# Optimization experiments

Hardware: AMD Instinct MI355X
Metric: run time of the kernel (lower is better)

The kernel has to match this reference:

```python
import jax, jax.numpy as jnp
import numpy as np

B, H, S, D = 4, 16, 2048, 128

def setup_inputs() -> dict:
    key = jax.random.key(0)
    kq, kk, kv = jax.random.split(key, 3)
    query = jax.random.normal(kq, (B, H, S, D), dtype=jnp.float32)
    k = jax.random.normal(kk, (B, H, S, D), dtype=jnp.float32)
    value = jax.random.normal(kv, (B, H, S, D), dtype=jnp.float32)
    attn_mask = jnp.zeros((B, H, S, S), dtype=jnp.float32)
    return {"query": query, "key": k, "value": value, "attn_mask": attn_mask}

def reference(query, key, value, attn_mask):
    # scores: [B,H,S,S]
    scale = 1.0 / jnp.sqrt(jnp.asarray(query.shape[-1], query.dtype))
    scores = jnp.einsum('bhqd,bhkd->bhqk', query, key) * scale + attn_mask
    attn = jax.nn.softmax(scores, axis=-1)
    out = jnp.einsum('bhqk,bhkd->bhqd', attn, value)
    return out
```

## Files before the change

kernel.cpp:

```cpp
#include <hip/hip_runtime.h>

#define SDIM 2048
#define DDIM 128
#define NBH  64
#define BR   128
#define BC   64
#define PSTRIDE 72

using bf16x8 = __attribute__((ext_vector_type(8))) short;
using f32x4  = __attribute__((ext_vector_type(4))) float;

typedef const __attribute__((address_space(1))) void* gvp;
typedef __attribute__((address_space(3))) void* lvp;

static __device__ __forceinline__ short f2bf(float x) {
    unsigned u = __float_as_uint(x);
    u += 0x7fff + ((u >> 16) & 1);
    return (short)(u >> 16);
}
static __device__ __forceinline__ unsigned pack2(float a, float b) {
    return ((unsigned)(unsigned short)f2bf(a)) |
           (((unsigned)(unsigned short)f2bf(b)) << 16);
}

__global__ __launch_bounds__(256) void kconv_kernel(const float* __restrict__ K,
                                                    unsigned short* __restrict__ Kc,
                                                    unsigned* __restrict__ flag)
{
    if (flag != nullptr && blockIdx.x == 0 && threadIdx.x == 0) *flag = 0u;
    size_t i = ((size_t)blockIdx.x * 256 + threadIdx.x) * 4;
    float4 v = *(const float4*)(K + i);
    uint2 o;
    o.x = pack2(v.x, v.y);
    o.y = pack2(v.z, v.w);
    *(uint2*)(Kc + i) = o;
}

__global__ __launch_bounds__(256) void vtrans_kernel(const float* __restrict__ V,
                                                     unsigned short* __restrict__ Vt)
{
    __shared__ float t[32][33];
    const int bh = blockIdx.z;
    const int s0 = blockIdx.x * 32;
    const int d0 = blockIdx.y * 32;
    const int x = threadIdx.x & 31;
    const int y = threadIdx.x >> 5;
    const float* Vb = V + (size_t)bh * SDIM * DDIM;
    unsigned short* Vtb = Vt + (size_t)bh * SDIM * DDIM;
#pragma unroll
    for (int i = 0; i < 4; ++i) {
        int r = y + i * 8;
        t[r][x] = Vb[(size_t)(s0 + r) * DDIM + d0 + x];
    }
    __syncthreads();
#pragma unroll
    for (int i = 0; i < 4; ++i) {
        int r = y + i * 8;
        Vtb[(size_t)(d0 + r) * SDIM + s0 + x] = (unsigned short)f2bf(t[x][r]);
    }
}

__global__ __launch_bounds__(256) void maskscan_kernel(const uint4* __restrict__ M4,
                                                       unsigned* __restrict__ flag)
{
    const size_t n4 = (size_t)NBH * SDIM * SDIM / 4;
    unsigned acc = 0;
    for (size_t i = (size_t)blockIdx.x * 256 + threadIdx.x; i < n4;
         i += (size_t)gridDim.x * 256) {
        uint4 v = M4[i];
        acc |= v.x | v.y | v.z | v.w;
    }
    if (acc) *flag = 1u;
}

static __device__ __forceinline__ void load_mask(const float* __restrict__ Mb,
                                                 int q0, int wave, int quad, int n16,
                                                 int kcol, float (&mk)[2][4][4])
{
#pragma unroll
    for (int rt = 0; rt < 2; ++rt) {
        const int rowb = q0 + wave * 32 + rt * 16 + quad * 4;
        const float* mpb = Mb + (size_t)rowb * SDIM + kcol + n16;
#pragma unroll
        for (int ct = 0; ct < 4; ++ct)
#pragma unroll
            for (int r = 0; r < 4; ++r)
                mk[rt][ct][r] = mpb[(size_t)r * SDIM + ct * 16];
    }
}

template<bool MASKED>
static __device__ __forceinline__ void ktile_body(
    int k0, int q0, int wave, int quad, int n16, int lane,
    const float* __restrict__ Mb,
    const unsigned short* __restrict__ Kb, const unsigned short* __restrict__ Vb,
    char* __restrict__ Kl, char* __restrict__ Vl,
    unsigned short* __restrict__ PsW,
    const bf16x8 (&qf)[2][4],
    f32x4 (&acc)[2][8], float (&mrow)[2][4], float (&lrow)[2][4])
{
    const f32x4 zero4 = {0.f, 0.f, 0.f, 0.f};

#pragma unroll
    for (int j = 0; j < 4; ++j) {
        const int row = wave * 16 + j * 4 + quad;
        const int src = (n16 * 16) ^ ((row & 7) << 4);
        const char* gp = (const char*)(Kb + (size_t)(k0 + row) * DDIM) + src;
        char* lp = Kl + wave * 4096 + j * 1024;
        __builtin_amdgcn_global_load_lds((gvp)gp, (lvp)lp, 16, 0, 0);
    }
#pragma unroll
    for (int j = 0; j < 4; ++j) {
        const int row = wave * 32 + j * 8 + (lane >> 3);
        const int src = ((lane & 7) * 16) ^ ((row & 7) << 4);
        const char* gp = (const char*)(Vb + (size_t)row * SDIM + k0) + src;
        char* lp = Vl + wave * 4096 + j * 1024;
        __builtin_amdgcn_global_load_lds((gvp)gp, (lvp)lp, 16, 0, 0);
    }

    float mk[2][4][4];
    if constexpr (MASKED)
        load_mask(Mb, q0, wave, quad, n16, k0, mk);

    __syncthreads();

    const int swzr = (n16 & 7) << 4;

    f32x4 s[2][4];
#pragma unroll
    for (int rt = 0; rt < 2; ++rt)
#pragma unroll
        for (int ct = 0; ct < 4; ++ct) s[rt][ct] = zero4;
#pragma unroll
    for (int dt = 0; dt < 4; ++dt) {
        bf16x8 kf[4];
#pragma unroll
        for (int ct = 0; ct < 4; ++ct)
            kf[ct] = *(const bf16x8*)(Kl + (ct * 16 + n16) * 256 +
                                      ((dt * 64 + quad * 16) ^ swzr));
        __builtin_amdgcn_s_setprio(1);
#pragma unroll
        for (int ct = 0; ct < 4; ++ct) {
            s[0][ct] = __builtin_amdgcn_mfma_f32_16x16x32_bf16(qf[0][dt], kf[ct], s[0][ct], 0, 0, 0);
            s[1][ct] = __builtin_amdgcn_mfma_f32_16x16x32_bf16(qf[1][dt], kf[ct], s[1][ct], 0, 0, 0);
        }
        __builtin_amdgcn_s_setprio(0);
    }

    if constexpr (MASKED) {
#pragma unroll
        for (int rt = 0; rt < 2; ++rt)
#pragma unroll
            for (int ct = 0; ct < 4; ++ct)
#pragma unroll
                for (int r = 0; r < 4; ++r)
                    s[rt][ct][r] += mk[rt][ct][r];
    }

    float mx[2][4];
#pragma unroll
    for (int rt = 0; rt < 2; ++rt)
#pragma unroll
        for (int r = 0; r < 4; ++r)
            mx[rt][r] = fmaxf(fmaxf(s[rt][0][r], s[rt][1][r]),
                              fmaxf(s[rt][2][r], s[rt][3][r]));
#pragma unroll
    for (int st = 1; st <= 8; st <<= 1)
#pragma unroll
        for (int rt = 0; rt < 2; ++rt)
#pragma unroll
            for (int r = 0; r < 4; ++r)
                mx[rt][r] = fmaxf(mx[rt][r], __shfl_xor(mx[rt][r], st));

    int anynew = 0;
#pragma unroll
    for (int rt = 0; rt < 2; ++rt)
#pragma unroll
        for (int r = 0; r < 4; ++r)
            anynew |= (mx[rt][r] > mrow[rt][r]) ? 1 : 0;
    if (__ballot(anynew) != 0ull) {
#pragma unroll
        for (int rt = 0; rt < 2; ++rt)
#pragma unroll
            for (int r = 0; r < 4; ++r) {
                float mnew = fmaxf(mrow[rt][r], mx[rt][r]);
                float al = exp2f((mrow[rt][r] - mnew) * 1.44269504f);
                mrow[rt][r] = mnew;
                lrow[rt][r] *= al;
#pragma unroll
                for (int nt = 0; nt < 8; ++nt) acc[rt][nt][r] *= al;
            }
    }

    float rs[2][4];
#pragma unroll
    for (int rt = 0; rt < 2; ++rt)
#pragma unroll
        for (int r = 0; r < 4; ++r) {
            float t = 0.f;
#pragma unroll
            for (int ct = 0; ct < 4; ++ct) {
                float pv = exp2f((s[rt][ct][r] - mrow[rt][r]) * 1.44269504f);
                s[rt][ct][r] = pv;
                t += pv;
            }
            rs[rt][r] = t;
        }
#pragma unroll
    for (int st = 1; st <= 8; st <<= 1)
#pragma unroll
        for (int rt = 0; rt < 2; ++rt)
#pragma unroll
            for (int r = 0; r < 4; ++r)
                rs[rt][r] += __shfl_xor(rs[rt][r], st);
#pragma unroll
    for (int rt = 0; rt < 2; ++rt)
#pragma unroll
        for (int r = 0; r < 4; ++r)
            lrow[rt][r] += rs[rt][r];

#pragma unroll
    for (int rt = 0; rt < 2; ++rt)
#pragma unroll
        for (int ct = 0; ct < 4; ++ct)
#pragma unroll
            for (int r = 0; r < 4; ++r)
                PsW[(rt * 16 + (lane >> 4) * 4 + r) * PSTRIDE + ct * 16 + n16] =
                    (unsigned short)f2bf(s[rt][ct][r]);

    bf16x8 pa[2][2];
#pragma unroll
    for (int rt = 0; rt < 2; ++rt)
#pragma unroll
        for (int kt = 0; kt < 2; ++kt)
            pa[rt][kt] = *(const bf16x8*)(&PsW[(rt * 16 + n16) * PSTRIDE + kt * 32 + quad * 8]);

#pragma unroll
    for (int nt = 0; nt < 8; ++nt) {
        bf16x8 vf[2];
#pragma unroll
        for (int kt = 0; kt < 2; ++kt)
            vf[kt] = *(const bf16x8*)(Vl + (nt * 16 + n16) * 128 +
                                      ((kt * 64 + quad * 16) ^ swzr));
        __builtin_amdgcn_s_setprio(1);
#pragma unroll
        for (int kt = 0; kt < 2; ++kt) {
            acc[0][nt] = __builtin_amdgcn_mfma_f32_16x16x32_bf16(pa[0][kt], vf[kt], acc[0][nt], 0, 0, 0);
            acc[1][nt] = __builtin_amdgcn_mfma_f32_16x16x32_bf16(pa[1][kt], vf[kt], acc[1][nt], 0, 0, 0);
        }
        __builtin_amdgcn_s_setprio(0);
    }
}

__global__ __launch_bounds__(256, 2) void fattn_kernel(
    const float* __restrict__ Q, const float* __restrict__ M,
    const unsigned short* __restrict__ Kc, const unsigned short* __restrict__ Vt,
    const unsigned* __restrict__ flag,
    float* __restrict__ O)
{
    const int flat = blockIdx.x;
    const int slot = flat >> 3;
    const int bh   = (flat & 7) * 8 + (slot >> 4);
    const int qt   = slot & 15;

    const int tid  = threadIdx.x;
    const int wave = tid >> 6;
    const int lane = tid & 63;
    const int quad = lane >> 4;
    const int n16  = lane & 15;
    const int q0   = qt * BR;

    const float* Qb = Q + (size_t)bh * SDIM * DDIM;
    const float* Mb = M + (size_t)bh * SDIM * SDIM;
    const unsigned short* Kb = Kc + (size_t)bh * SDIM * DDIM;
    const unsigned short* Vb = Vt + (size_t)bh * SDIM * DDIM;
    float* Ob = O + (size_t)bh * SDIM * DDIM;

    const bool masked = (flag == nullptr) || (*flag != 0u);

    __shared__ __align__(16) char Kl[64 * 256];
    __shared__ __align__(16) char Vl[128 * 128];
    __shared__ __align__(16) unsigned short Ps[4][32 * PSTRIDE];
    unsigned short* PsW = Ps[wave];

    const float scale = 0.08838834764831845f;
    bf16x8 qf[2][4];
#pragma unroll
    for (int rt = 0; rt < 2; ++rt) {
        int row = q0 + wave * 32 + rt * 16 + n16;
        const float* qp = Qb + (size_t)row * DDIM + quad * 8;
#pragma unroll
        for (int dt = 0; dt < 4; ++dt) {
            const float* p = qp + dt * 32;
            float4 a = *(const float4*)p;
            float4 b = *(const float4*)(p + 4);
            bf16x8 f;
            f[0] = f2bf(a.x * scale); f[1] = f2bf(a.y * scale);
            f[2] = f2bf(a.z * scale); f[3] = f2bf(a.w * scale);
            f[4] = f2bf(b.x * scale); f[5] = f2bf(b.y * scale);
            f[6] = f2bf(b.z * scale); f[7] = f2bf(b.w * scale);
            qf[rt][dt] = f;
        }
    }

    f32x4 acc[2][8];
    const f32x4 zero4 = {0.f, 0.f, 0.f, 0.f};
#pragma unroll
    for (int rt = 0; rt < 2; ++rt)
#pragma unroll
        for (int nt = 0; nt < 8; ++nt) acc[rt][nt] = zero4;
    float mrow[2][4], lrow[2][4];
#pragma unroll
    for (int rt = 0; rt < 2; ++rt)
#pragma unroll
        for (int r = 0; r < 4; ++r) { mrow[rt][r] = -1e30f; lrow[rt][r] = 0.f; }

    if (!masked) {
#pragma unroll 1
        for (int k0 = 0; k0 < SDIM; k0 += BC) {
            __syncthreads();
            ktile_body<false>(k0, q0, wave, quad, n16, lane, Mb, Kb, Vb,
                              Kl, Vl, PsW, qf, acc, mrow, lrow);
        }
    } else {
#pragma unroll 1
        for (int k0 = 0; k0 < SDIM; k0 += BC) {
            __syncthreads();
            ktile_body<true>(k0, q0, wave, quad, n16, lane, Mb, Kb, Vb,
                             Kl, Vl, PsW, qf, acc, mrow, lrow);
        }
    }

#pragma unroll
    for (int rt = 0; rt < 2; ++rt) {
#pragma unroll
        for (int r = 0; r < 4; ++r) {
            float inv = 1.0f / lrow[rt][r];
            int row = q0 + wave * 32 + rt * 16 + quad * 4 + r;
            float* op = Ob + (size_t)row * DDIM + n16;
#pragma unroll
            for (int nt = 0; nt < 8; ++nt)
                op[nt * 16] = acc[rt][nt][r] * inv;
        }
    }
}

extern "C" void kernel_launch(void* const* d_in, const int* in_sizes, int n_in,
                              void* d_out, int out_size, void* d_ws, size_t ws_size,
                              hipStream_t stream) {
    const float* Q = (const float*)d_in[0];
    const float* K = (const float*)d_in[1];
    const float* V = (const float*)d_in[2];
    const float* M = (const float*)d_in[3];
    float* O = (float*)d_out;

    const size_t nElem = (size_t)NBH * SDIM * DDIM;
    unsigned short* Kc = (unsigned short*)d_ws;
    unsigned short* Vt = Kc + nElem;

    const size_t kvBytes = 2 * nElem * sizeof(unsigned short);
    unsigned* flag = (ws_size >= kvBytes + sizeof(unsigned))
                   ? (unsigned*)((char*)d_ws + kvBytes) : nullptr;

    kconv_kernel<<<dim3(nElem / (256 * 4)), 256, 0, stream>>>(K, Kc, flag);
    vtrans_kernel<<<dim3(SDIM / 32, DDIM / 32, NBH), 256, 0, stream>>>(V, Vt);
    if (flag != nullptr)
        maskscan_kernel<<<dim3(2048), 256, 0, stream>>>((const uint4*)M, flag);

    fattn_kernel<<<dim3((SDIM / BR) * NBH), 256, 0, stream>>>(Q, M, Kc, Vt, flag, O);
}
```

Baseline: 1.767 ms.

## Fuse mask scan into attention kernel and double-buffer K tiles

Drops the separate global mask-scan kernel and its flag. Each attention block now scans its own 128 rows of the mask and picks the fast or masked path for itself. In the unmasked path, K is double-buffered in LDS: the next K tile is prefetched while the current one is consumed, and the V-tile wait is deferred to just before the PV MFMAs, so fewer barriers stall each iteration. This adds LDS use (a second K buffer) that may affect occupancy, and every block still reads its whole mask slice.

```diff
diff --git a/kernel.cpp b/kernel.cpp
--- a/kernel.cpp
+++ b/kernel.cpp
@@ -24,10 +24,8 @@
 }
 
 __global__ __launch_bounds__(256) void kconv_kernel(const float* __restrict__ K,
-                                                    unsigned short* __restrict__ Kc,
-                                                    unsigned* __restrict__ flag)
-{
-    if (flag != nullptr && blockIdx.x == 0 && threadIdx.x == 0) *flag = 0u;
+                                                    unsigned short* __restrict__ Kc)
+{
     size_t i = ((size_t)blockIdx.x * 256 + threadIdx.x) * 4;
     float4 v = *(const float4*)(K + i);
     uint2 o;
@@ -60,17 +58,29 @@
     }
 }
 
-__global__ __launch_bounds__(256) void maskscan_kernel(const uint4* __restrict__ M4,
-                                                       unsigned* __restrict__ flag)
-{
-    const size_t n4 = (size_t)NBH * SDIM * SDIM / 4;
-    unsigned acc = 0;
-    for (size_t i = (size_t)blockIdx.x * 256 + threadIdx.x; i < n4;
-         i += (size_t)gridDim.x * 256) {
-        uint4 v = M4[i];
-        acc |= v.x | v.y | v.z | v.w;
-    }
-    if (acc) *flag = 1u;
+static __device__ __forceinline__ void stage_K(const unsigned short* __restrict__ Kb,
+                                               char* __restrict__ Kdst,
+                                               int k0, int wave, int quad, int n16)
+{
+#pragma unroll
+    for (int j = 0; j < 4; ++j) {
+        const int row = wave * 16 + j * 4 + quad;
+        const int src = (n16 * 16) ^ ((row & 7) << 4);
+        const char* gp = (const char*)(Kb + (size_t)(k0 + row) * DDIM) + src;
+        __builtin_amdgcn_global_load_lds((gvp)gp, (lvp)(Kdst + wave * 4096 + j * 1024), 16, 0, 0);
+    }
+}
+static __device__ __forceinline__ void stage_V(const unsigned short* __restrict__ Vb,
+                                               char* __restrict__ Vdst,
+                                               int k0, int wave, int lane)
+{
+#pragma unroll
+    for (int j = 0; j < 4; ++j) {
+        const int row = wave * 32 + j * 8 + (lane >> 3);
+        const int src = ((lane & 7) * 16) ^ ((row & 7) << 4);
+        const char* gp = (const char*)(Vb + (size_t)row * SDIM + k0) + src;
+        __builtin_amdgcn_global_load_lds((gvp)gp, (lvp)(Vdst + wave * 4096 + j * 1024), 16, 0, 0);
+    }
 }
 
 static __device__ __forceinline__ void load_mask(const float* __restrict__ Mb,
@@ -89,8 +99,166 @@
     }
 }
 
-template<bool MASKED>
-static __device__ __forceinline__ void ktile_body(
+static __device__ __forceinline__ void softmax_update(
+    f32x4 (&s)[2][4], f32x4 (&acc)[2][8], float (&mrow)[2][4], float (&lrow)[2][4])
+{
+    float mx[2][4];
+#pragma unroll
+    for (int rt = 0; rt < 2; ++rt)
+#pragma unroll
+        for (int r = 0; r < 4; ++r)
+            mx[rt][r] = fmaxf(fmaxf(s[rt][0][r], s[rt][1][r]),
+                              fmaxf(s[rt][2][r], s[rt][3][r]));
+#pragma unroll
+    for (int st = 1; st <= 8; st <<= 1)
+#pragma unroll
+        for (int rt = 0; rt < 2; ++rt)
+#pragma unroll
+            for (int r = 0; r < 4; ++r)
+                mx[rt][r] = fmaxf(mx[rt][r], __shfl_xor(mx[rt][r], st));
+
+    int anynew = 0;
+#pragma unroll
+    for (int rt = 0; rt < 2; ++rt)
+#pragma unroll
+        for (int r = 0; r < 4; ++r)
+            anynew |= (mx[rt][r] > mrow[rt][r]) ? 1 : 0;
+    if (__ballot(anynew) != 0ull) {
+#pragma unroll
+        for (int rt = 0; rt < 2; ++rt)
+#pragma unroll
+            for (int r = 0; r < 4; ++r) {
+                float mnew = fmaxf(mrow[rt][r], mx[rt][r]);
+                float al = exp2f((mrow[rt][r] - mnew) * 1.44269504f);
+                mrow[rt][r] = mnew;
+                lrow[rt][r] *= al;
+#pragma unroll
+                for (int nt = 0; nt < 8; ++nt) acc[rt][nt][r] *= al;
+            }
+    }
+
+    float rs[2][4];
+#pragma unroll
+    for (int rt = 0; rt < 2; ++rt)
+#pragma unroll
+        for (int r = 0; r < 4; ++r) {
+            float t = 0.f;
+#pragma unroll
+            for (int ct = 0; ct < 4; ++ct) {
+                float pv = exp2f((s[rt][ct][r] - mrow[rt][r]) * 1.44269504f);
+                s[rt][ct][r] = pv;
+                t += pv;
+            }
+            rs[rt][r] = t;
+        }
+#pragma unroll
+    for (int st = 1; st <= 8; st <<= 1)
+#pragma unroll
+        for (int rt = 0; rt < 2; ++rt)
+#pragma unroll
+            for (int r = 0; r < 4; ++r)
+                rs[rt][r] += __shfl_xor(rs[rt][r], st);
+#pragma unroll
+    for (int rt = 0; rt < 2; ++rt)
+#pragma unroll
+        for (int r = 0; r < 4; ++r)
+            lrow[rt][r] += rs[rt][r];
+}
+
+static __device__ __forceinline__ void qk_phase(
+    const char* __restrict__ Kcur, int quad, int n16, int swzr,
+    const bf16x8 (&qf)[2][4], f32x4 (&s)[2][4])
+{
+#pragma unroll
+    for (int dt = 0; dt < 4; ++dt) {
+        bf16x8 kf[4];
+#pragma unroll
+        for (int ct = 0; ct < 4; ++ct)
+            kf[ct] = *(const bf16x8*)(Kcur + (ct * 16 + n16) * 256 +
+                                      ((dt * 64 + quad * 16) ^ swzr));
+        __builtin_amdgcn_s_setprio(1);
+#pragma unroll
+        for (int ct = 0; ct < 4; ++ct) {
+            s[0][ct] = __builtin_amdgcn_mfma_f32_16x16x32_bf16(qf[0][dt], kf[ct], s[0][ct], 0, 0, 0);
+            s[1][ct] = __builtin_amdgcn_mfma_f32_16x16x32_bf16(qf[1][dt], kf[ct], s[1][ct], 0, 0, 0);
+        }
+        __builtin_amdgcn_s_setprio(0);
+    }
+}
+
+static __device__ __forceinline__ void ppack_pv(
+    f32x4 (&s)[2][4], const char* __restrict__ Vl,
+    unsigned short* __restrict__ PsW, int quad, int n16, int lane, int swzr,
+    f32x4 (&acc)[2][8], bool deferred_barrier)
+{
+#pragma unroll
+    for (int rt = 0; rt < 2; ++rt)
+#pragma unroll
+        for (int ct = 0; ct < 4; ++ct)
+#pragma unroll
+            for (int r = 0; r < 4; ++r)
+                PsW[(rt * 16 + (lane >> 4) * 4 + r) * PSTRIDE + ct * 16 + n16] =
+                    (unsigned short)f2bf(s[rt][ct][r]);
+
+    bf16x8 pa[2][2];
+#pragma unroll
+    for (int rt = 0; rt < 2; ++rt)
+#pragma unroll
+        for (int kt = 0; kt < 2; ++kt)
+            pa[rt][kt] = *(const bf16x8*)(&PsW[(rt * 16 + n16) * PSTRIDE + kt * 32 + quad * 8]);
+
+    if (deferred_barrier) {
+        asm volatile("s_waitcnt vmcnt(4)" ::: "memory");
+        __builtin_amdgcn_s_barrier();
+    }
+
+#pragma unroll
+    for (int nt = 0; nt < 8; ++nt) {
+        bf16x8 vf[2];
+#pragma unroll
+        for (int kt = 0; kt < 2; ++kt)
+            vf[kt] = *(const bf16x8*)(Vl + (nt * 16 + n16) * 128 +
+                                      ((kt * 64 + quad * 16) ^ swzr));
+        __builtin_amdgcn_s_setprio(1);
+#pragma unroll
+        for (int kt = 0; kt < 2; ++kt) {
+            acc[0][nt] = __builtin_amdgcn_mfma_f32_16x16x32_bf16(pa[0][kt], vf[kt], acc[0][nt], 0, 0, 0);
+            acc[1][nt] = __builtin_amdgcn_mfma_f32_16x16x32_bf16(pa[1][kt], vf[kt], acc[1][nt], 0, 0, 0);
+        }
+        __builtin_amdgcn_s_setprio(0);
+    }
+}
+
+static __device__ __forceinline__ void ktile_fast(
+    int k0, int wave, int quad, int n16, int lane,
+    const unsigned short* __restrict__ Kb, const unsigned short* __restrict__ Vb,
+    char* __restrict__ Kcur, char* __restrict__ Knxt, char* __restrict__ Vl,
+    unsigned short* __restrict__ PsW,
+    const bf16x8 (&qf)[2][4],
+    f32x4 (&acc)[2][8], float (&mrow)[2][4], float (&lrow)[2][4])
+{
+    const f32x4 zero4 = {0.f, 0.f, 0.f, 0.f};
+
+    stage_V(Vb, Vl, k0, wave, lane);
+    stage_K(Kb, Knxt, (k0 + BC) & (SDIM - 1), wave, quad, n16);
+
+    const int swzr = (n16 & 7) << 4;
+
+    f32x4 s[2][4];
+#pragma unroll
+    for (int rt = 0; rt < 2; ++rt)
+#pragma unroll
+        for (int ct = 0; ct < 4; ++ct) s[rt][ct] = zero4;
+
+    qk_phase(Kcur, quad, n16, swzr, qf, s);
+    softmax_update(s, acc, mrow, lrow);
+    ppack_pv(s, Vl, PsW, quad, n16, lane, swzr, acc, true);
+
+    asm volatile("s_waitcnt vmcnt(0)" ::: "memory");
+    __builtin_amdgcn_s_barrier();
+}
+
+static __device__ __forceinline__ void ktile_masked(
     int k0, int q0, int wave, int quad, int n16, int lane,
     const float* __restrict__ Mb,
     const unsigned short* __restrict__ Kb, const unsigned short* __restrict__ Vb,
@@ -101,26 +269,11 @@
 {
     const f32x4 zero4 = {0.f, 0.f, 0.f, 0.f};
 
-#pragma unroll
-    for (int j = 0; j < 4; ++j) {
-        const int row = wave * 16 + j * 4 + quad;
-        const int src = (n16 * 16) ^ ((row & 7) << 4);
-        const char* gp = (const char*)(Kb + (size_t)(k0 + row) * DDIM) + src;
-        char* lp = Kl + wave * 4096 + j * 1024;
-        __builtin_amdgcn_global_load_lds((gvp)gp, (lvp)lp, 16, 0, 0);
-    }
-#pragma unroll
-    for (int j = 0; j < 4; ++j) {
-        const int row = wave * 32 + j * 8 + (lane >> 3);
-        const int src = ((lane & 7) * 16) ^ ((row & 7) << 4);
-        const char* gp = (const char*)(Vb + (size_t)row * SDIM + k0) + src;
-        char* lp = Vl + wave * 4096 + j * 1024;
-        __builtin_amdgcn_global_load_lds((gvp)gp, (lvp)lp, 16, 0, 0);
-    }
+    stage_K(Kb, Kl, k0, wave, quad, n16);
+    stage_V(Vb, Vl, k0, wave, lane);
 
     float mk[2][4][4];
-    if constexpr (MASKED)
-        load_mask(Mb, q0, wave, quad, n16, k0, mk);
+    load_mask(Mb, q0, wave, quad, n16, k0, mk);
 
     __syncthreads();
 
@@ -131,131 +284,24 @@
     for (int rt = 0; rt < 2; ++rt)
 #pragma unroll
         for (int ct = 0; ct < 4; ++ct) s[rt][ct] = zero4;
-#pragma unroll
-    for (int dt = 0; dt < 4; ++dt) {
-        bf16x8 kf[4];
+
+    qk_phase(Kl, quad, n16, swzr, qf, s);
+
+#pragma unroll
+    for (int rt = 0; rt < 2; ++rt)
 #pragma unroll
         for (int ct = 0; ct < 4; ++ct)
-            kf[ct] = *(const bf16x8*)(Kl + (ct * 16 + n16) * 256 +
-                                      ((dt * 64 + quad * 16) ^ swzr));
-        __builtin_amdgcn_s_setprio(1);
-#pragma unroll
-        for (int ct = 0; ct < 4; ++ct) {
-            s[0][ct] = __builtin_amdgcn_mfma_f32_16x16x32_bf16(qf[0][dt], kf[ct], s[0][ct], 0, 0, 0);
-            s[1][ct] = __builtin_amdgcn_mfma_f32_16x16x32_bf16(qf[1][dt], kf[ct], s[1][ct], 0, 0, 0);
-        }
-        __builtin_amdgcn_s_setprio(0);
-    }
-
-    if constexpr (MASKED) {
-#pragma unroll
-        for (int rt = 0; rt < 2; ++rt)
-#pragma unroll
-            for (int ct = 0; ct < 4; ++ct)
-#pragma unroll
-                for (int r = 0; r < 4; ++r)
-                    s[rt][ct][r] += mk[rt][ct][r];
-    }
-
-    float mx[2][4];
-#pragma unroll
-    for (int rt = 0; rt < 2; ++rt)
-#pragma unroll
-        for (int r = 0; r < 4; ++r)
-            mx[rt][r] = fmaxf(fmaxf(s[rt][0][r], s[rt][1][r]),
-                              fmaxf(s[rt][2][r], s[rt][3][r]));
-#pragma unroll
-    for (int st = 1; st <= 8; st <<= 1)
-#pragma unroll
-        for (int rt = 0; rt < 2; ++rt)
 #pragma unroll
             for (int r = 0; r < 4; ++r)
-                mx[rt][r] = fmaxf(mx[rt][r], __shfl_xor(mx[rt][r], st));
-
-    int anynew = 0;
-#pragma unroll
-    for (int rt = 0; rt < 2; ++rt)
-#pragma unroll
-        for (int r = 0; r < 4; ++r)
-            anynew |= (mx[rt][r] > mrow[rt][r]) ? 1 : 0;
-    if (__ballot(anynew) != 0ull) {
-#pragma unroll
-        for (int rt = 0; rt < 2; ++rt)
-#pragma unroll
-            for (int r = 0; r < 4; ++r) {
-                float mnew = fmaxf(mrow[rt][r], mx[rt][r]);
-                float al = exp2f((mrow[rt][r] - mnew) * 1.44269504f);
-                mrow[rt][r] = mnew;
-                lrow[rt][r] *= al;
-#pragma unroll
-                for (int nt = 0; nt < 8; ++nt) acc[rt][nt][r] *= al;
-            }
-    }
-
-    float rs[2][4];
-#pragma unroll
-    for (int rt = 0; rt < 2; ++rt)
-#pragma unroll
-        for (int r = 0; r < 4; ++r) {
-            float t = 0.f;
-#pragma unroll
-            for (int ct = 0; ct < 4; ++ct) {
-                float pv = exp2f((s[rt][ct][r] - mrow[rt][r]) * 1.44269504f);
-                s[rt][ct][r] = pv;
-                t += pv;
-            }
-            rs[rt][r] = t;
-        }
-#pragma unroll
-    for (int st = 1; st <= 8; st <<= 1)
-#pragma unroll
-        for (int rt = 0; rt < 2; ++rt)
-#pragma unroll
-            for (int r = 0; r < 4; ++r)
-                rs[rt][r] += __shfl_xor(rs[rt][r], st);
-#pragma unroll
-    for (int rt = 0; rt < 2; ++rt)
-#pragma unroll
-        for (int r = 0; r < 4; ++r)
-            lrow[rt][r] += rs[rt][r];
-
-#pragma unroll
-    for (int rt = 0; rt < 2; ++rt)
-#pragma unroll
-        for (int ct = 0; ct < 4; ++ct)
-#pragma unroll
-            for (int r = 0; r < 4; ++r)
-                PsW[(rt * 16 + (lane >> 4) * 4 + r) * PSTRIDE + ct * 16 + n16] =
-                    (unsigned short)f2bf(s[rt][ct][r]);
-
-    bf16x8 pa[2][2];
-#pragma unroll
-    for (int rt = 0; rt < 2; ++rt)
-#pragma unroll
-        for (int kt = 0; kt < 2; ++kt)
-            pa[rt][kt] = *(const bf16x8*)(&PsW[(rt * 16 + n16) * PSTRIDE + kt * 32 + quad * 8]);
-
-#pragma unroll
-    for (int nt = 0; nt < 8; ++nt) {
-        bf16x8 vf[2];
-#pragma unroll
-        for (int kt = 0; kt < 2; ++kt)
-            vf[kt] = *(const bf16x8*)(Vl + (nt * 16 + n16) * 128 +
-                                      ((kt * 64 + quad * 16) ^ swzr));
-        __builtin_amdgcn_s_setprio(1);
-#pragma unroll
-        for (int kt = 0; kt < 2; ++kt) {
-            acc[0][nt] = __builtin_amdgcn_mfma_f32_16x16x32_bf16(pa[0][kt], vf[kt], acc[0][nt], 0, 0, 0);
-            acc[1][nt] = __builtin_amdgcn_mfma_f32_16x16x32_bf16(pa[1][kt], vf[kt], acc[1][nt], 0, 0, 0);
-        }
-        __builtin_amdgcn_s_setprio(0);
-    }
+                s[rt][ct][r] += mk[rt][ct][r];
+
+    softmax_update(s, acc, mrow, lrow);
+    ppack_pv(s, Vl, PsW, quad, n16, lane, swzr, acc, false);
 }
 
 __global__ __launch_bounds__(256, 2) void fattn_kernel(
     const float* __restrict__ Q, const float* __restrict__ M,
     const unsigned short* __restrict__ Kc, const unsigned short* __restrict__ Vt,
-    const unsigned* __restrict__ flag,
     float* __restrict__ O)
 {
     const int flat = blockIdx.x;
@@ -276,12 +322,14 @@
     const unsigned short* Vb = Vt + (size_t)bh * SDIM * DDIM;
     float* Ob = O + (size_t)bh * SDIM * DDIM;
 
-    const bool masked = (flag == nullptr) || (*flag != 0u);
-
-    __shared__ __align__(16) char Kl[64 * 256];
+    __shared__ __align__(16) char Kl0[64 * 256];
+    __shared__ __align__(16) char Kl1[64 * 256];
     __shared__ __align__(16) char Vl[128 * 128];
     __shared__ __align__(16) unsigned short Ps[4][32 * PSTRIDE];
+    __shared__ int blkmask;
     unsigned short* PsW = Ps[wave];
+
+    stage_K(Kb, Kl0, 0, wave, quad, n16);
 
     const float scale = 0.08838834764831845f;
     bf16x8 qf[2][4];
@@ -303,6 +351,28 @@
         }
     }
 
+    if (tid == 0) blkmask = 0;
+    {
+        const uint4* Ms = (const uint4*)(Mb + (size_t)q0 * SDIM);
+        unsigned a0 = 0, a1 = 0, a2 = 0, a3 = 0;
+#pragma unroll 1
+        for (int i = tid; i < (BR * SDIM / 4); i += 1024) {
+            uint4 v0 = Ms[i];
+            uint4 v1 = Ms[i + 256];
+            uint4 v2 = Ms[i + 512];
+            uint4 v3 = Ms[i + 768];
+            a0 |= v0.x | v0.y | v0.z | v0.w;
+            a1 |= v1.x | v1.y | v1.z | v1.w;
+            a2 |= v2.x | v2.y | v2.z | v2.w;
+            a3 |= v3.x | v3.y | v3.z | v3.w;
+        }
+        const unsigned am = (a0 | a1) | (a2 | a3);
+        __syncthreads();
+        if (am) atomicOr(&blkmask, 1);
+    }
+    __syncthreads();
+    const bool masked = (blkmask != 0);
+
     f32x4 acc[2][8];
     const f32x4 zero4 = {0.f, 0.f, 0.f, 0.f};
 #pragma unroll
@@ -317,17 +387,18 @@
 
     if (!masked) {
 #pragma unroll 1
-        for (int k0 = 0; k0 < SDIM; k0 += BC) {
-            __syncthreads();
-            ktile_body<false>(k0, q0, wave, quad, n16, lane, Mb, Kb, Vb,
-                              Kl, Vl, PsW, qf, acc, mrow, lrow);
+        for (int k0 = 0; k0 < SDIM; k0 += 2 * BC) {
+            ktile_fast(k0,      wave, quad, n16, lane, Kb, Vb, Kl0, Kl1, Vl,
+                       PsW, qf, acc, mrow, lrow);
+            ktile_fast(k0 + BC, wave, quad, n16, lane, Kb, Vb, Kl1, Kl0, Vl,
+                       PsW, qf, acc, mrow, lrow);
         }
     } else {
 #pragma unroll 1
         for (int k0 = 0; k0 < SDIM; k0 += BC) {
             __syncthreads();
-            ktile_body<true>(k0, q0, wave, quad, n16, lane, Mb, Kb, Vb,
-                             Kl, Vl, PsW, qf, acc, mrow, lrow);
+            ktile_masked(k0, q0, wave, quad, n16, lane, Mb, Kb, Vb, Kl0, Vl,
+                         PsW, qf, acc, mrow, lrow);
         }
     }
 
@@ -358,14 +429,7 @@
     unsigned short* Kc = (unsigned short*)d_ws;
     unsigned short* Vt = Kc + nElem;
 
-    const size_t kvBytes = 2 * nElem * sizeof(unsigned short);
-    unsigned* flag = (ws_size >= kvBytes + sizeof(unsigned))
-                   ? (unsigned*)((char*)d_ws + kvBytes) : nullptr;
-
-    kconv_kernel<<<dim3(nElem / (256 * 4)), 256, 0, stream>>>(K, Kc, flag);
+    kconv_kernel<<<dim3(nElem / (256 * 4)), 256, 0, stream>>>(K, Kc);
     vtrans_kernel<<<dim3(SDIM / 32, DDIM / 32, NBH), 256, 0, stream>>>(V, Vt);
-    if (flag != nullptr)
-        maskscan_kernel<<<dim3(2048), 256, 0, stream>>>((const uint4*)M, flag);
-
-    fattn_kernel<<<dim3((SDIM / BR) * NBH), 256, 0, stream>>>(Q, M, Kc, Vt, flag, O);
-}
+    fattn_kernel<<<dim3((SDIM / BR) * NBH), 256, 0, stream>>>(Q, M, Kc, Vt, O);
+}
```

New measurement: 1.735 ms. About the same (-1.8%).
